# Performance work log

Hardware: AMD Instinct MI355X
Metric: run time of the kernel (lower is better)

The kernel has to match this reference:

```python
import jax, jax.numpy as jnp
import numpy as np

N_NODE = 1_000_000
N_BOND = 100_000
K_TWIST = 40
MAX_ORDER = 8
N_DOMAIN = 10_000
SIGMA_MAX = float(np.pi)  # config.sigma_max (=1) * pi


def setup_inputs() -> dict:
    key = jax.random.key(0)
    k1, k2, k3, k4, k5 = jax.random.split(key, 5)
    pos = jax.random.normal(k1, (N_NODE, 3), jnp.float32) * 10.0
    info_level = jax.random.uniform(k2, (N_BOND,), jnp.float32)
    # bond annotation: [order, u, v]
    uv = jax.random.randint(k3, (N_BOND, 2), 0, N_NODE, dtype=jnp.int32)
    order = (jnp.arange(N_BOND, dtype=jnp.int32) % MAX_ORDER)
    tor_bonds_anno = jnp.concatenate([order[:, None], uv], axis=1)
    # twisted nodes: bond b (order b%MAX_ORDER, group g=b//MAX_ORDER) twists
    # nodes g*K_TWIST .. g*K_TWIST+K_TWIST-1  -> disjoint within each order level
    b = jnp.arange(N_BOND, dtype=jnp.int32)
    nodes = (b // MAX_ORDER)[:, None] * K_TWIST + jnp.arange(K_TWIST, dtype=jnp.int32)[None, :]
    index_tor = jnp.repeat(b, K_TWIST)
    twisted_nodes_anno = jnp.stack([index_tor, nodes.reshape(-1)], axis=1)
    # rigid domains: contiguous blocks of nodes
    node_index = jnp.arange(N_NODE, dtype=jnp.int32)
    domain_index = node_index // (N_NODE // N_DOMAIN)
    eps = jax.random.normal(k4, (N_BOND,), jnp.float32)
    uniform_angles = jax.random.uniform(k5, (N_BOND,), jnp.float32, minval=-np.pi, maxval=np.pi)
    return {
        "pos": pos, "info_level": info_level,
        "tor_bonds_anno": tor_bonds_anno, "twisted_nodes_anno": twisted_nodes_anno,
        "domain_index": domain_index, "node_index": node_index,
        "eps": eps, "uniform_angles": uniform_angles, "from_prior": 1,
    }


def _rodrigues(axis, angle):
    # axis: [B,3] unit vectors, angle: [B] -> R: [B,3,3]
    c = jnp.cos(angle)[:, None, None]
    s = jnp.sin(angle)[:, None, None]
    ax, ay, az = axis[:, 0], axis[:, 1], axis[:, 2]
    zero = jnp.zeros_like(ax)
    K = jnp.stack([
        jnp.stack([zero, -az, ay], -1),
        jnp.stack([az, zero, -ax], -1),
        jnp.stack([-ay, ax, zero], -1),
    ], axis=1)  # [B,3,3]
    aaT = axis[:, :, None] * axis[:, None, :]
    I = jnp.eye(3, dtype=axis.dtype)[None]
    return c * I + s * K + (1.0 - c) * aaT


def _torsion_and_kabsch(pos, info_level, eps, uniform_angles,
                        tor_bonds_anno, twisted_nodes_anno,
                        domain_index, node_index, from_prior):
    tor_order = tor_bonds_anno[:, 0]
    u, v = tor_bonds_anno[:, 1], tor_bonds_anno[:, 2]
    index_tor = twisted_nodes_anno[:, 0]
    tnodes = twisted_nodes_anno[:, 1]

    sigmas = (1.0 - info_level) * SIGMA_MAX
    angles_wn = eps * sigmas  # wrapped-normal sample (rotation is 2pi-periodic)
    if from_prior:
        angles = jnp.where(info_level == 0, uniform_angles, angles_wn)
    else:
        angles = angles_wn

    pos_tor = pos
    # sequential application by torsion order (axes move as parents rotate)
    for o in range(MAX_ORDER):
        axis_raw = pos_tor[v] - pos_tor[u]
        axis = axis_raw / (jnp.linalg.norm(axis_raw, axis=-1, keepdims=True) + 1e-12)
        R = _rodrigues(axis, angles)                      # [n_bond,3,3]
        pivot = pos_tor[v]                                # rotate about atom v on the axis
        p = pos_tor[tnodes] - pivot[index_tor]            # [n_twisted,3]
        rot = jnp.einsum('nij,nj->ni', R[index_tor], p) + pivot[index_tor]
        mask = (tor_order[index_tor] == o)[:, None]
        delta = jnp.where(mask, rot - pos_tor[tnodes], 0.0)
        pos_tor = pos_tor.at[tnodes].add(delta)

    # decouple: per-domain Kabsch alignment of pos_tor back onto pos
    P = pos_tor[node_index]
    Q = pos[node_index]
    cnt = jax.ops.segment_sum(jnp.ones((P.shape[0],), P.dtype), domain_index, N_DOMAIN)[:, None]
    cP = jax.ops.segment_sum(P, domain_index, N_DOMAIN) / cnt
    cQ = jax.ops.segment_sum(Q, domain_index, N_DOMAIN) / cnt
    Pc = P - cP[domain_index]
    Qc = Q - cQ[domain_index]
    H = jax.ops.segment_sum(Pc[:, :, None] * Qc[:, None, :], domain_index, N_DOMAIN)  # [D,3,3]
    Uh, S, Vt = jnp.linalg.svd(H)
    V = jnp.swapaxes(Vt, 1, 2)
    d = jnp.sign(jnp.linalg.det(jnp.matmul(V, jnp.swapaxes(Uh, 1, 2))))  # [D]
    Vm = jnp.concatenate([V[:, :, :2], V[:, :, 2:] * d[:, None, None]], axis=2)
    Rg = jnp.matmul(Vm, jnp.swapaxes(Uh, 1, 2))            # [D,3,3], Rg @ p ~ q
    tg = cQ - jnp.einsum('dij,dj->di', Rg, cP)             # [D,3]
    corrected = jnp.einsum('nij,nj->ni', Rg[domain_index], P) + tg[domain_index]
    return pos_tor.at[node_index].set(corrected)


def reference(pos, info_level, tor_bonds_anno, twisted_nodes_anno,
              domain_index, node_index, eps, uniform_angles, from_prior):
    return _torsion_and_kabsch(pos, info_level, eps, uniform_angles,
                               tor_bonds_anno, twisted_nodes_anno,
                               domain_index, node_index, from_prior)
```

## Files before the change

kernel.cpp:

```cpp
#include <hip/hip_runtime.h>
#include <math.h>

#define N_NODE    1000000
#define N_BOND    100000
#define K_TWIST   40
#define MAX_ORDER 8
#define N_DOMAIN  10000
#define N_PER_DOM 100
#define N_GROUP   12500
#define N_TWIST   500000
#define SIGMA_MAXF 3.14159265358979323846f


#define M0_OFF  1500000
#define M1_OFF  1650000
#define BP_OFF  1800000

__global__ __launch_bounds__(256) void gather_k(
    const float* __restrict__ pos, const float* __restrict__ info_level,
    const int* __restrict__ anno, const float* __restrict__ eps,
    const float* __restrict__ uni, const int* __restrict__ from_prior_p,
    float* __restrict__ out)
{
    int b = blockIdx.x * 256 + threadIdx.x;
    if (b >= N_BOND) return;
    int o = b & (MAX_ORDER - 1);
    int u = anno[3*b + 1];
    int v = anno[3*b + 2];
    float info = info_level[b];
    float ang  = eps[b] * (1.0f - info) * SIGMA_MAXF;
    if (from_prior_p[0] != 0 && info == 0.0f) ang = uni[b];
    float4 r0, r1, r2;
    r0.x = pos[3*u+0]; r0.y = pos[3*u+1]; r0.z = pos[3*u+2];
    r0.w = pos[3*v+0]; r1.x = pos[3*v+1]; r1.y = pos[3*v+2];
    r1.z = cosf(ang);  r1.w = sinf(ang);
    r2.x = (u < N_TWIST) ? (float)(u / K_TWIST) : -1.0f;
    r2.y = (v < N_TWIST) ? (float)(v / K_TWIST) : -1.0f;
    r2.z = (anno[3*b] == o) ? 1.0f : 0.0f;
    r2.w = 0.0f;
    float4* bp4 = (float4*)(out + BP_OFF);
    bp4[3*b + 0] = r0;
    bp4[3*b + 1] = r1;
    bp4[3*b + 2] = r2;
}

__global__ __launch_bounds__(256) void compose_k(float* __restrict__ out, int o)
{
    int g = blockIdx.x * 256 + threadIdx.x;
    if (g >= N_GROUP) return;
    const float4* bp4 = (const float4*)(out + BP_OFF);
    const float* Mp = out + ((o & 1) ? M0_OFF : M1_OFF);
    float*       Mc = out + ((o & 1) ? M1_OFF : M0_OFF);
    int b = g * MAX_ORDER + o;
    float4 r0 = bp4[3*b + 0];
    float4 r1 = bp4[3*b + 1];
    float4 r2 = bp4[3*b + 2];
    float* mg = Mc + 12 * g;
    if (r2.z == 0.0f) {
        if (o == 0) {
            mg[0]=1.f; mg[1]=0.f; mg[2]=0.f;
            mg[3]=0.f; mg[4]=1.f; mg[5]=0.f;
            mg[6]=0.f; mg[7]=0.f; mg[8]=1.f;
            mg[9]=0.f; mg[10]=0.f; mg[11]=0.f;
        } else {
            const float* mp = Mp + 12 * g;
            #pragma unroll
            for (int k = 0; k < 12; k++) mg[k] = mp[k];
        }
        return;
    }
    float pu0 = r0.x, pu1 = r0.y, pu2 = r0.z;
    float pv0 = r0.w, pv1 = r1.x, pv2 = r1.y;
    float c = r1.z, s = r1.w;
    if (o > 0) {
        int gu = (int)r2.x;
        int gv = (int)r2.y;
        if (gu >= 0) {
            const float* m = Mp + 12 * gu;
            float a0 = m[0]*pu0 + m[1]*pu1 + m[2]*pu2 + m[9];
            float a1 = m[3]*pu0 + m[4]*pu1 + m[5]*pu2 + m[10];
            float a2 = m[6]*pu0 + m[7]*pu1 + m[8]*pu2 + m[11];
            pu0 = a0; pu1 = a1; pu2 = a2;
        }
        if (gv >= 0) {
            const float* m = Mp + 12 * gv;
            float a0 = m[0]*pv0 + m[1]*pv1 + m[2]*pv2 + m[9];
            float a1 = m[3]*pv0 + m[4]*pv1 + m[5]*pv2 + m[10];
            float a2 = m[6]*pv0 + m[7]*pv1 + m[8]*pv2 + m[11];
            pv0 = a0; pv1 = a1; pv2 = a2;
        }
    }
    float ax = pv0-pu0, ay = pv1-pu1, az = pv2-pu2;
    float inv = 1.0f / (sqrtf(ax*ax + ay*ay + az*az) + 1e-12f);
    ax *= inv; ay *= inv; az *= inv;
    float t = 1.0f - c;
    float R00 = c + t*ax*ax,     R01 = -s*az + t*ax*ay, R02 =  s*ay + t*ax*az;
    float R10 =  s*az + t*ay*ax, R11 = c + t*ay*ay,     R12 = -s*ax + t*ay*az;
    float R20 = -s*ay + t*az*ax, R21 =  s*ax + t*az*ay, R22 = c + t*az*az;
    if (o == 0) {
        mg[0]=R00; mg[1]=R01; mg[2]=R02;
        mg[3]=R10; mg[4]=R11; mg[5]=R12;
        mg[6]=R20; mg[7]=R21; mg[8]=R22;
        mg[9]  = pv0 - (R00*pv0 + R01*pv1 + R02*pv2);
        mg[10] = pv1 - (R10*pv0 + R11*pv1 + R12*pv2);
        mg[11] = pv2 - (R20*pv0 + R21*pv1 + R22*pv2);
    } else {
        const float* mp = Mp + 12 * g;
        mg[0] = R00*mp[0] + R01*mp[3] + R02*mp[6];
        mg[1] = R00*mp[1] + R01*mp[4] + R02*mp[7];
        mg[2] = R00*mp[2] + R01*mp[5] + R02*mp[8];
        mg[3] = R10*mp[0] + R11*mp[3] + R12*mp[6];
        mg[4] = R10*mp[1] + R11*mp[4] + R12*mp[7];
        mg[5] = R10*mp[2] + R11*mp[5] + R12*mp[8];
        mg[6] = R20*mp[0] + R21*mp[3] + R22*mp[6];
        mg[7] = R20*mp[1] + R21*mp[4] + R22*mp[7];
        mg[8] = R20*mp[2] + R21*mp[5] + R22*mp[8];
        float d0 = mp[9]-pv0, d1 = mp[10]-pv1, d2 = mp[11]-pv2;
        mg[9]  = R00*d0 + R01*d1 + R02*d2 + pv0;
        mg[10] = R10*d0 + R11*d1 + R12*d2 + pv1;
        mg[11] = R20*d0 + R21*d1 + R22*d2 + pv2;
    }
}

__device__ inline void cross3d(const double a[3], const double b[3], double r[3])
{
    r[0] = a[1]*b[2] - a[2]*b[1];
    r[1] = a[2]*b[0] - a[0]*b[2];
    r[2] = a[0]*b[1] - a[1]*b[0];
}

__device__ void kabsch_from_sums(const float* s, float* __restrict__ rt)
{
    const double inv_n = 1.0 / (double)N_PER_DOM;
    double sP[3] = { s[0], s[1], s[2] };
    double sQ[3] = { s[3], s[4], s[5] };
    double H[3][3];
    #pragma unroll
    for (int i = 0; i < 3; i++)
        #pragma unroll
        for (int j = 0; j < 3; j++)
            H[i][j] = (double)s[6 + 3*i + j] - sP[i]*sQ[j]*inv_n;
    double A[3][3];
    #pragma unroll
    for (int i = 0; i < 3; i++)
        #pragma unroll
        for (int j = 0; j < 3; j++)
            A[i][j] = H[0][i]*H[0][j] + H[1][i]*H[1][j] + H[2][i]*H[2][j];
    double V[3][3] = {{1,0,0},{0,1,0},{0,0,1}};
    for (int sweep = 0; sweep < 30; sweep++) {
        double off = A[0][1]*A[0][1] + A[0][2]*A[0][2] + A[1][2]*A[1][2];
        double n2  = A[0][0]*A[0][0] + A[1][1]*A[1][1] + A[2][2]*A[2][2];
        if (off <= 1e-28 * n2) break;
        for (int pp = 0; pp < 3; pp++) {
            int p = (pp == 2) ? 1 : 0;
            int q = (pp == 0) ? 1 : 2;
            double apq = A[p][q];
            if (apq == 0.0) continue;
            double tau = (A[q][q] - A[p][p]) / (2.0 * apq);
            double tj  = (tau >= 0.0 ? 1.0 : -1.0) / (fabs(tau) + sqrt(1.0 + tau*tau));
            double cj  = 1.0 / sqrt(1.0 + tj*tj);
            double sj  = tj * cj;
            int r = 3 - p - q;
            double app = A[p][p], aqq = A[q][q];
            A[p][p] = app - tj*apq;
            A[q][q] = aqq + tj*apq;
            A[p][q] = 0.0; A[q][p] = 0.0;
            double arp = A[r][p], arq = A[r][q];
            A[r][p] = cj*arp - sj*arq; A[p][r] = A[r][p];
            A[r][q] = sj*arp + cj*arq; A[q][r] = A[r][q];
            #pragma unroll
            for (int k = 0; k < 3; k++) {
                double vp = V[k][p], vq = V[k][q];
                V[k][p] = cj*vp - sj*vq;
                V[k][q] = sj*vp + cj*vq;
            }
        }
    }
    double wv[3] = { A[0][0], A[1][1], A[2][2] };
    int i0 = 0, i1 = 1, i2 = 2;
    if (wv[i0] < wv[i1]) { int t = i0; i0 = i1; i1 = t; }
    if (wv[i0] < wv[i2]) { int t = i0; i0 = i2; i2 = t; }
    if (wv[i1] < wv[i2]) { int t = i1; i1 = i2; i2 = t; }
    double v0[3] = { V[0][i0], V[1][i0], V[2][i0] };
    double v1[3] = { V[0][i1], V[1][i1], V[2][i1] };
    double v2[3] = { V[0][i2], V[1][i2], V[2][i2] };
    double s0 = sqrt(fmax(wv[i0], 0.0));
    double Rg[3][3];
    if (s0 < 1e-200) {
        Rg[0][0]=1; Rg[0][1]=0; Rg[0][2]=0;
        Rg[1][0]=0; Rg[1][1]=1; Rg[1][2]=0;
        Rg[2][0]=0; Rg[2][1]=0; Rg[2][2]=1;
    } else {
        double u0[3], u1[3], u2[3];
        #pragma unroll
        for (int i = 0; i < 3; i++)
            u0[i] = H[i][0]*v0[0] + H[i][1]*v0[1] + H[i][2]*v0[2];
        double n0 = sqrt(u0[0]*u0[0] + u0[1]*u0[1] + u0[2]*u0[2]);
        if (n0 > 0.0) { u0[0]/=n0; u0[1]/=n0; u0[2]/=n0; }
        else { u0[0]=1; u0[1]=0; u0[2]=0; }
        #pragma unroll
        for (int i = 0; i < 3; i++)
            u1[i] = H[i][0]*v1[0] + H[i][1]*v1[1] + H[i][2]*v1[2];
        double dp = u0[0]*u1[0] + u0[1]*u1[1] + u0[2]*u1[2];
        u1[0] -= dp*u0[0]; u1[1] -= dp*u0[1]; u1[2] -= dp*u0[2];
        double n1 = sqrt(u1[0]*u1[0] + u1[1]*u1[1] + u1[2]*u1[2]);
        if (n1 > 1e-12 * n0) { u1[0]/=n1; u1[1]/=n1; u1[2]/=n1; }
        else {
            double tv[3] = { (fabs(u0[0]) < 0.9) ? 1.0 : 0.0,
                             (fabs(u0[0]) < 0.9) ? 0.0 : 1.0, 0.0 };
            cross3d(u0, tv, u1);
            double nn = sqrt(u1[0]*u1[0] + u1[1]*u1[1] + u1[2]*u1[2]);
            u1[0]/=nn; u1[1]/=nn; u1[2]/=nn;
        }
        cross3d(u0, u1, u2);
        double c12[3]; cross3d(v1, v2, c12);
        double detV = v0[0]*c12[0] + v0[1]*c12[1] + v0[2]*c12[2];
        double dsg = (detV >= 0.0) ? 1.0 : -1.0;
        #pragma unroll
        for (int r = 0; r < 3; r++)
            #pragma unroll
            for (int c = 0; c < 3; c++)
                Rg[r][c] = v0[r]*u0[c] + v1[r]*u1[c] + dsg*v2[r]*u2[c];
    }
    double cP[3] = { sP[0]*inv_n, sP[1]*inv_n, sP[2]*inv_n };
    double cQ[3] = { sQ[0]*inv_n, sQ[1]*inv_n, sQ[2]*inv_n };
    #pragma unroll
    for (int i = 0; i < 3; i++) {
        rt[3*i+0] = (float)Rg[i][0];
        rt[3*i+1] = (float)Rg[i][1];
        rt[3*i+2] = (float)Rg[i][2];
        rt[9+i] = (float)(cQ[i] - (Rg[i][0]*cP[0] + Rg[i][1]*cP[1] + Rg[i][2]*cP[2]));
    }
}

__device__ inline void acc15(float a[15], float p0, float p1, float p2,
                             float q0, float q1, float q2)
{
    a[0]+=p0;    a[1]+=p1;    a[2]+=p2;
    a[3]+=q0;    a[4]+=q1;    a[5]+=q2;
    a[6]+=p0*q0; a[7]+=p0*q1; a[8]+=p0*q2;
    a[9]+=p1*q0; a[10]+=p1*q1;a[11]+=p1*q2;
    a[12]+=p2*q0;a[13]+=p2*q1;a[14]+=p2*q2;
}

__global__ __launch_bounds__(256) void rsvd_k(const float* __restrict__ pos,
                                              const float* __restrict__ out,
                                              float* __restrict__ rt)
{
    int d = blockIdx.x * 256 + threadIdx.x;
    if (d >= N_DOMAIN) return;
    const float4* pv4 = (const float4*)pos;
    const float* Mf = out + M1_OFF;
    float a[15];
    #pragma unroll
    for (int k = 0; k < 15; k++) a[k] = 0.f;

    if (d >= N_TWIST / N_PER_DOM) {
        int base = 75 * d;
        for (int c = 0; c < 25; c++) {
            float4 f0 = pv4[base + 3*c + 0];
            float4 f1 = pv4[base + 3*c + 1];
            float4 f2 = pv4[base + 3*c + 2];
            acc15(a, f0.x, f0.y, f0.z, f0.x, f0.y, f0.z);
            acc15(a, f0.w, f1.x, f1.y, f0.w, f1.x, f1.y);
            acc15(a, f1.z, f1.w, f2.x, f1.z, f1.w, f2.x);
            acc15(a, f2.y, f2.z, f2.w, f2.y, f2.z, f2.w);
        }
    } else {
        int n = d * N_PER_DOM, end = n + N_PER_DOM;
        while (n < end) {
            int g = n / K_TWIST;
            int segEnd = min(end, K_TWIST * (g + 1));
            const float* m = Mf + 12 * g;
            float m0=m[0],m1=m[1],m2=m[2],m3=m[3],m4=m[4],m5=m[5];
            float m6=m[6],m7=m[7],m8=m[8],m9=m[9],m10=m[10],m11=m[11];
            int chunks = (segEnd - n) >> 2;
            int base = (3 * n) >> 2;
            for (int c = 0; c < chunks; c++) {
                float4 f0 = pv4[base + 3*c + 0];
                float4 f1 = pv4[base + 3*c + 1];
                float4 f2 = pv4[base + 3*c + 2];
                float q0, q1, q2, p0, p1, p2;
                q0=f0.x; q1=f0.y; q2=f0.z;
                p0=m0*q0+m1*q1+m2*q2+m9; p1=m3*q0+m4*q1+m5*q2+m10; p2=m6*q0+m7*q1+m8*q2+m11;
                acc15(a, p0, p1, p2, q0, q1, q2);
                q0=f0.w; q1=f1.x; q2=f1.y;
                p0=m0*q0+m1*q1+m2*q2+m9; p1=m3*q0+m4*q1+m5*q2+m10; p2=m6*q0+m7*q1+m8*q2+m11;
                acc15(a, p0, p1, p2, q0, q1, q2);
                q0=f1.z; q1=f1.w; q2=f2.x;
                p0=m0*q0+m1*q1+m2*q2+m9; p1=m3*q0+m4*q1+m5*q2+m10; p2=m6*q0+m7*q1+m8*q2+m11;
                acc15(a, p0, p1, p2, q0, q1, q2);
                q0=f2.y; q1=f2.z; q2=f2.w;
                p0=m0*q0+m1*q1+m2*q2+m9; p1=m3*q0+m4*q1+m5*q2+m10; p2=m6*q0+m7*q1+m8*q2+m11;
                acc15(a, p0, p1, p2, q0, q1, q2);
            }
            n = segEnd;
        }
    }
    kabsch_from_sums(a, rt + (size_t)d * 12);
}

__global__ void apply_low_k(const float* __restrict__ pos,
                            const float* __restrict__ rt,
                            float* __restrict__ out)
{
    int n = blockIdx.x * 256 + threadIdx.x;
    if (n >= N_TWIST) return;
    const float* m = out + M1_OFF + 12 * (n / K_TWIST);
    const float* w = rt + 12 * (n / N_PER_DOM);
    float q0 = pos[3*n+0], q1 = pos[3*n+1], q2 = pos[3*n+2];
    float p0 = m[0]*q0 + m[1]*q1 + m[2]*q2 + m[9];
    float p1 = m[3]*q0 + m[4]*q1 + m[5]*q2 + m[10];
    float p2 = m[6]*q0 + m[7]*q1 + m[8]*q2 + m[11];
    out[3*n+0] = w[0]*p0 + w[1]*p1 + w[2]*p2 + w[9];
    out[3*n+1] = w[3]*p0 + w[4]*p1 + w[5]*p2 + w[10];
    out[3*n+2] = w[6]*p0 + w[7]*p1 + w[8]*p2 + w[11];
}

__global__ void apply_high_k(const float* __restrict__ pos,
                             const float* __restrict__ rt,
                             float* __restrict__ out)
{
    int i = blockIdx.x * 256 + threadIdx.x;
    int n = N_TWIST + i;
    if (n >= N_NODE) return;
    const float* w = rt + 12 * (n / N_PER_DOM);
    float q0 = pos[3*n+0], q1 = pos[3*n+1], q2 = pos[3*n+2];
    out[3*n+0] = w[0]*q0 + w[1]*q1 + w[2]*q2 + w[9];
    out[3*n+1] = w[3]*q0 + w[4]*q1 + w[5]*q2 + w[10];
    out[3*n+2] = w[6]*q0 + w[7]*q1 + w[8]*q2 + w[11];
}

extern "C" void kernel_launch(void* const* d_in, const int* in_sizes, int n_in,
                              void* d_out, int out_size, void* d_ws, size_t ws_size,
                              hipStream_t stream)
{
    const float* pos        = (const float*)d_in[0];
    const float* info_level = (const float*)d_in[1];
    const int*   anno       = (const int*)  d_in[2];
    const float* eps        = (const float*)d_in[6];
    const float* uni        = (const float*)d_in[7];
    const int*   from_prior = (const int*)  d_in[8];
    float* out = (float*)d_out;
    float* rt  = (float*)d_ws;

    gather_k<<<(N_BOND + 255)/256, 256, 0, stream>>>(
        pos, info_level, anno, eps, uni, from_prior, out);

    for (int o = 0; o < MAX_ORDER; o++)
        compose_k<<<(N_GROUP + 255)/256, 256, 0, stream>>>(out, o);

    rsvd_k<<<(N_DOMAIN + 255)/256, 256, 0, stream>>>(pos, out, rt);

    apply_low_k<<<(N_TWIST + 255)/256, 256, 0, stream>>>(pos, rt, out);
    apply_high_k<<<(N_NODE - N_TWIST + 255)/256, 256, 0, stream>>>(pos, rt, out);
}
```

Baseline: 186.3 us.

## Fuse per-order compose launches into one dataflow kernel with spin flags

Replaces the eight sequential compose kernel launches with a single kernel in which each group thread iterates over all orders. Cross-group dependencies are resolved through per-group progress flags, spin-waited with atomics, and each order level's matrices are stored in a separate buffer. This removes seven launches and their inter-kernel gaps, at the cost of atomic traffic and a deadlock risk if dependent groups are not co-resident. The buffer layout moves to per-level storage, and the final level feeds the downstream kernels.

Result: slower. 205.7 us (+10.4%).

```diff
diff --git a/kernel.cpp b/kernel.cpp
--- a/kernel.cpp
+++ b/kernel.cpp
@@ -12,18 +12,21 @@
 #define SIGMA_MAXF 3.14159265358979323846f
 
 
-#define M0_OFF  1500000
-#define M1_OFF  1650000
-#define BP_OFF  1800000
+#define BP_OFF   0
+#define MLV_OFF  1500000
+#define MLV_STRIDE 150000
+#define RT_WORDS 120000
+#define SPIN_MAX 100000000
 
 __global__ __launch_bounds__(256) void gather_k(
     const float* __restrict__ pos, const float* __restrict__ info_level,
     const int* __restrict__ anno, const float* __restrict__ eps,
     const float* __restrict__ uni, const int* __restrict__ from_prior_p,
-    float* __restrict__ out)
+    float* __restrict__ out, unsigned int* __restrict__ flags)
 {
     int b = blockIdx.x * 256 + threadIdx.x;
     if (b >= N_BOND) return;
+    if (b < N_GROUP) atomicExch(&flags[b], 0u);
     int o = b & (MAX_ORDER - 1);
     int u = anno[3*b + 1];
     int v = anno[3*b + 2];
@@ -44,81 +47,122 @@
     bp4[3*b + 2] = r2;
 }
 
-__global__ __launch_bounds__(256) void compose_k(float* __restrict__ out, int o)
+__device__ inline unsigned long long pack2f(float a, float b)
+{
+    return ((unsigned long long)__float_as_uint(b) << 32) | __float_as_uint(a);
+}
+
+__device__ inline void unpack2f(unsigned long long w, float* a, float* b)
+{
+    *a = __uint_as_float((unsigned int)(w & 0xffffffffull));
+    *b = __uint_as_float((unsigned int)(w >> 32));
+}
+
+__device__ inline void spin_flag(unsigned int* f, unsigned int need)
+{
+    for (int it = 0; it < SPIN_MAX; ++it)
+        if (atomicAdd(f, 0u) >= need) return;
+}
+
+__device__ inline void read_M(unsigned long long* mp, float m[12])
+{
+    unsigned long long w0 = atomicAdd(&mp[0], 0ull);
+    unsigned long long w1 = atomicAdd(&mp[1], 0ull);
+    unsigned long long w2 = atomicAdd(&mp[2], 0ull);
+    unsigned long long w3 = atomicAdd(&mp[3], 0ull);
+    unsigned long long w4 = atomicAdd(&mp[4], 0ull);
+    unsigned long long w5 = atomicAdd(&mp[5], 0ull);
+    unpack2f(w0, &m[0], &m[1]);  unpack2f(w1, &m[2], &m[3]);
+    unpack2f(w2, &m[4], &m[5]);  unpack2f(w3, &m[6], &m[7]);
+    unpack2f(w4, &m[8], &m[9]);  unpack2f(w5, &m[10], &m[11]);
+}
+
+__global__ __launch_bounds__(256) void compose_df_k(float* __restrict__ out,
+                                                    unsigned int* __restrict__ flags)
 {
     int g = blockIdx.x * 256 + threadIdx.x;
     if (g >= N_GROUP) return;
     const float4* bp4 = (const float4*)(out + BP_OFF);
-    const float* Mp = out + ((o & 1) ? M0_OFF : M1_OFF);
-    float*       Mc = out + ((o & 1) ? M1_OFF : M0_OFF);
-    int b = g * MAX_ORDER + o;
-    float4 r0 = bp4[3*b + 0];
-    float4 r1 = bp4[3*b + 1];
-    float4 r2 = bp4[3*b + 2];
-    float* mg = Mc + 12 * g;
-    if (r2.z == 0.0f) {
-        if (o == 0) {
-            mg[0]=1.f; mg[1]=0.f; mg[2]=0.f;
-            mg[3]=0.f; mg[4]=1.f; mg[5]=0.f;
-            mg[6]=0.f; mg[7]=0.f; mg[8]=1.f;
-            mg[9]=0.f; mg[10]=0.f; mg[11]=0.f;
-        } else {
-            const float* mp = Mp + 12 * g;
-            #pragma unroll
-            for (int k = 0; k < 12; k++) mg[k] = mp[k];
+    float M[12];
+    for (int o = 0; o < MAX_ORDER; o++) {
+        int b = g * MAX_ORDER + o;
+        float4 r0 = bp4[3*b + 0];
+        float4 r1 = bp4[3*b + 1];
+        float4 r2 = bp4[3*b + 2];
+        if (r2.z != 0.0f) {
+            float pu0 = r0.x, pu1 = r0.y, pu2 = r0.z;
+            float pv0 = r0.w, pv1 = r1.x, pv2 = r1.y;
+            float c = r1.z, s = r1.w;
+            if (o > 0) {
+                int gu = (int)r2.x;
+                int gv = (int)r2.y;
+                unsigned long long* Mprev =
+                    (unsigned long long*)(out + MLV_OFF + (size_t)(o-1) * MLV_STRIDE);
+                if (gu >= 0) {
+                    spin_flag(&flags[gu], (unsigned int)o);
+                    float m[12];
+                    read_M(Mprev + 6 * gu, m);
+                    float a0 = m[0]*pu0 + m[1]*pu1 + m[2]*pu2 + m[9];
+                    float a1 = m[3]*pu0 + m[4]*pu1 + m[5]*pu2 + m[10];
+                    float a2 = m[6]*pu0 + m[7]*pu1 + m[8]*pu2 + m[11];
+                    pu0 = a0; pu1 = a1; pu2 = a2;
+                }
+                if (gv >= 0) {
+                    spin_flag(&flags[gv], (unsigned int)o);
+                    float m[12];
+                    read_M(Mprev + 6 * gv, m);
+                    float a0 = m[0]*pv0 + m[1]*pv1 + m[2]*pv2 + m[9];
+                    float a1 = m[3]*pv0 + m[4]*pv1 + m[5]*pv2 + m[10];
+                    float a2 = m[6]*pv0 + m[7]*pv1 + m[8]*pv2 + m[11];
+                    pv0 = a0; pv1 = a1; pv2 = a2;
+                }
+            }
+            float ax = pv0-pu0, ay = pv1-pu1, az = pv2-pu2;
+            float inv = 1.0f / (sqrtf(ax*ax + ay*ay + az*az) + 1e-12f);
+            ax *= inv; ay *= inv; az *= inv;
+            float t = 1.0f - c;
+            float R00 = c + t*ax*ax,     R01 = -s*az + t*ax*ay, R02 =  s*ay + t*ax*az;
+            float R10 =  s*az + t*ay*ax, R11 = c + t*ay*ay,     R12 = -s*ax + t*ay*az;
+            float R20 = -s*ay + t*az*ax, R21 =  s*ax + t*az*ay, R22 = c + t*az*az;
+            if (o == 0) {
+                M[0]=R00; M[1]=R01; M[2]=R02;
+                M[3]=R10; M[4]=R11; M[5]=R12;
+                M[6]=R20; M[7]=R21; M[8]=R22;
+                M[9]  = pv0 - (R00*pv0 + R01*pv1 + R02*pv2);
+                M[10] = pv1 - (R10*pv0 + R11*pv1 + R12*pv2);
+                M[11] = pv2 - (R20*pv0 + R21*pv1 + R22*pv2);
+            } else {
+                float n0 = R00*M[0] + R01*M[3] + R02*M[6];
+                float n1 = R00*M[1] + R01*M[4] + R02*M[7];
+                float n2 = R00*M[2] + R01*M[5] + R02*M[8];
+                float n3 = R10*M[0] + R11*M[3] + R12*M[6];
+                float n4 = R10*M[1] + R11*M[4] + R12*M[7];
+                float n5 = R10*M[2] + R11*M[5] + R12*M[8];
+                float n6 = R20*M[0] + R21*M[3] + R22*M[6];
+                float n7 = R20*M[1] + R21*M[4] + R22*M[7];
+                float n8 = R20*M[2] + R21*M[5] + R22*M[8];
+                float d0 = M[9]-pv0, d1 = M[10]-pv1, d2 = M[11]-pv2;
+                float n9  = R00*d0 + R01*d1 + R02*d2 + pv0;
+                float n10 = R10*d0 + R11*d1 + R12*d2 + pv1;
+                float n11 = R20*d0 + R21*d1 + R22*d2 + pv2;
+                M[0]=n0; M[1]=n1; M[2]=n2; M[3]=n3; M[4]=n4; M[5]=n5;
+                M[6]=n6; M[7]=n7; M[8]=n8; M[9]=n9; M[10]=n10; M[11]=n11;
+            }
+        } else if (o == 0) {
+            M[0]=1.f; M[1]=0.f; M[2]=0.f; M[3]=0.f; M[4]=1.f; M[5]=0.f;
+            M[6]=0.f; M[7]=0.f; M[8]=1.f; M[9]=0.f; M[10]=0.f; M[11]=0.f;
         }
-        return;
-    }
-    float pu0 = r0.x, pu1 = r0.y, pu2 = r0.z;
-    float pv0 = r0.w, pv1 = r1.x, pv2 = r1.y;
-    float c = r1.z, s = r1.w;
-    if (o > 0) {
-        int gu = (int)r2.x;
-        int gv = (int)r2.y;
-        if (gu >= 0) {
-            const float* m = Mp + 12 * gu;
-            float a0 = m[0]*pu0 + m[1]*pu1 + m[2]*pu2 + m[9];
-            float a1 = m[3]*pu0 + m[4]*pu1 + m[5]*pu2 + m[10];
-            float a2 = m[6]*pu0 + m[7]*pu1 + m[8]*pu2 + m[11];
-            pu0 = a0; pu1 = a1; pu2 = a2;
-        }
-        if (gv >= 0) {
-            const float* m = Mp + 12 * gv;
-            float a0 = m[0]*pv0 + m[1]*pv1 + m[2]*pv2 + m[9];
-            float a1 = m[3]*pv0 + m[4]*pv1 + m[5]*pv2 + m[10];
-            float a2 = m[6]*pv0 + m[7]*pv1 + m[8]*pv2 + m[11];
-            pv0 = a0; pv1 = a1; pv2 = a2;
-        }
-    }
-    float ax = pv0-pu0, ay = pv1-pu1, az = pv2-pu2;
-    float inv = 1.0f / (sqrtf(ax*ax + ay*ay + az*az) + 1e-12f);
-    ax *= inv; ay *= inv; az *= inv;
-    float t = 1.0f - c;
-    float R00 = c + t*ax*ax,     R01 = -s*az + t*ax*ay, R02 =  s*ay + t*ax*az;
-    float R10 =  s*az + t*ay*ax, R11 = c + t*ay*ay,     R12 = -s*ax + t*ay*az;
-    float R20 = -s*ay + t*az*ax, R21 =  s*ax + t*az*ay, R22 = c + t*az*az;
-    if (o == 0) {
-        mg[0]=R00; mg[1]=R01; mg[2]=R02;
-        mg[3]=R10; mg[4]=R11; mg[5]=R12;
-        mg[6]=R20; mg[7]=R21; mg[8]=R22;
-        mg[9]  = pv0 - (R00*pv0 + R01*pv1 + R02*pv2);
-        mg[10] = pv1 - (R10*pv0 + R11*pv1 + R12*pv2);
-        mg[11] = pv2 - (R20*pv0 + R21*pv1 + R22*pv2);
-    } else {
-        const float* mp = Mp + 12 * g;
-        mg[0] = R00*mp[0] + R01*mp[3] + R02*mp[6];
-        mg[1] = R00*mp[1] + R01*mp[4] + R02*mp[7];
-        mg[2] = R00*mp[2] + R01*mp[5] + R02*mp[8];
-        mg[3] = R10*mp[0] + R11*mp[3] + R12*mp[6];
-        mg[4] = R10*mp[1] + R11*mp[4] + R12*mp[7];
-        mg[5] = R10*mp[2] + R11*mp[5] + R12*mp[8];
-        mg[6] = R20*mp[0] + R21*mp[3] + R22*mp[6];
-        mg[7] = R20*mp[1] + R21*mp[4] + R22*mp[7];
-        mg[8] = R20*mp[2] + R21*mp[5] + R22*mp[8];
-        float d0 = mp[9]-pv0, d1 = mp[10]-pv1, d2 = mp[11]-pv2;
-        mg[9]  = R00*d0 + R01*d1 + R02*d2 + pv0;
-        mg[10] = R10*d0 + R11*d1 + R12*d2 + pv1;
-        mg[11] = R20*d0 + R21*d1 + R22*d2 + pv2;
+
+        unsigned long long* mp =
+            (unsigned long long*)(out + MLV_OFF + (size_t)o * MLV_STRIDE) + 6 * g;
+        atomicExch(&mp[0], pack2f(M[0], M[1]));
+        atomicExch(&mp[1], pack2f(M[2], M[3]));
+        atomicExch(&mp[2], pack2f(M[4], M[5]));
+        atomicExch(&mp[3], pack2f(M[6], M[7]));
+        atomicExch(&mp[4], pack2f(M[8], M[9]));
+        atomicExch(&mp[5], pack2f(M[10], M[11]));
+        __threadfence();
+        atomicExch(&flags[g], (unsigned int)(o + 1));
     }
 }
 
@@ -250,7 +294,7 @@
     int d = blockIdx.x * 256 + threadIdx.x;
     if (d >= N_DOMAIN) return;
     const float4* pv4 = (const float4*)pos;
-    const float* Mf = out + M1_OFF;
+    const float* Mf = out + MLV_OFF + 7 * MLV_STRIDE;
     float a[15];
     #pragma unroll
     for (int k = 0; k < 15; k++) a[k] = 0.f;
@@ -306,7 +350,7 @@
 {
     int n = blockIdx.x * 256 + threadIdx.x;
     if (n >= N_TWIST) return;
-    const float* m = out + M1_OFF + 12 * (n / K_TWIST);
+    const float* m = out + MLV_OFF + 7 * MLV_STRIDE + 12 * (n / K_TWIST);
     const float* w = rt + 12 * (n / N_PER_DOM);
     float q0 = pos[3*n+0], q1 = pos[3*n+1], q2 = pos[3*n+2];
     float p0 = m[0]*q0 + m[1]*q1 + m[2]*q2 + m[9];
@@ -343,12 +387,12 @@
     const int*   from_prior = (const int*)  d_in[8];
     float* out = (float*)d_out;
     float* rt  = (float*)d_ws;
+    unsigned int* flags = (unsigned int*)((char*)d_ws + 480000);
 
     gather_k<<<(N_BOND + 255)/256, 256, 0, stream>>>(
-        pos, info_level, anno, eps, uni, from_prior, out);
-
-    for (int o = 0; o < MAX_ORDER; o++)
-        compose_k<<<(N_GROUP + 255)/256, 256, 0, stream>>>(out, o);
+        pos, info_level, anno, eps, uni, from_prior, out, flags);
+
+    compose_df_k<<<(N_GROUP + 255)/256, 256, 0, stream>>>(out, flags);
 
     rsvd_k<<<(N_DOMAIN + 255)/256, 256, 0, stream>>>(pos, out, rt);
 
```

## Fuse bond gather into compose and fold final order into consumers

Applied to the files above, without the earlier changes.

Removes the separate bond-parameter gather kernel, so each compose pass reads anno, pos and angle inputs directly and computes cos/sin only for active bonds. The last compose launch (order 7) is dropped; its transform is recomputed on the fly inside rsvd_k and apply_low_k from the order-6 matrices. rsvd_k now uses 64-thread blocks to spread the 10k domain threads over more blocks. This saves two launches and the staging buffer traffic, at the cost of redundant order-7 recomputation (one per node in apply_low_k) and heavier per-thread register use in rsvd_k.

After: 192.5 us. +3.3%, slower.

```diff
diff --git a/kernel.cpp b/kernel.cpp
--- a/kernel.cpp
+++ b/kernel.cpp
@@ -12,51 +12,22 @@
 #define SIGMA_MAXF 3.14159265358979323846f
 
 
-#define M0_OFF  1500000
-#define M1_OFF  1650000
-#define BP_OFF  1800000
-
-__global__ __launch_bounds__(256) void gather_k(
+#define TA_OFF  1500000
+#define TB_OFF  1650000
+
+__global__ __launch_bounds__(256) void compose_k(
     const float* __restrict__ pos, const float* __restrict__ info_level,
     const int* __restrict__ anno, const float* __restrict__ eps,
     const float* __restrict__ uni, const int* __restrict__ from_prior_p,
-    float* __restrict__ out)
-{
-    int b = blockIdx.x * 256 + threadIdx.x;
-    if (b >= N_BOND) return;
-    int o = b & (MAX_ORDER - 1);
-    int u = anno[3*b + 1];
-    int v = anno[3*b + 2];
-    float info = info_level[b];
-    float ang  = eps[b] * (1.0f - info) * SIGMA_MAXF;
-    if (from_prior_p[0] != 0 && info == 0.0f) ang = uni[b];
-    float4 r0, r1, r2;
-    r0.x = pos[3*u+0]; r0.y = pos[3*u+1]; r0.z = pos[3*u+2];
-    r0.w = pos[3*v+0]; r1.x = pos[3*v+1]; r1.y = pos[3*v+2];
-    r1.z = cosf(ang);  r1.w = sinf(ang);
-    r2.x = (u < N_TWIST) ? (float)(u / K_TWIST) : -1.0f;
-    r2.y = (v < N_TWIST) ? (float)(v / K_TWIST) : -1.0f;
-    r2.z = (anno[3*b] == o) ? 1.0f : 0.0f;
-    r2.w = 0.0f;
-    float4* bp4 = (float4*)(out + BP_OFF);
-    bp4[3*b + 0] = r0;
-    bp4[3*b + 1] = r1;
-    bp4[3*b + 2] = r2;
-}
-
-__global__ __launch_bounds__(256) void compose_k(float* __restrict__ out, int o)
+    float* __restrict__ out, int o)
 {
     int g = blockIdx.x * 256 + threadIdx.x;
     if (g >= N_GROUP) return;
-    const float4* bp4 = (const float4*)(out + BP_OFF);
-    const float* Mp = out + ((o & 1) ? M0_OFF : M1_OFF);
-    float*       Mc = out + ((o & 1) ? M1_OFF : M0_OFF);
+    const float* Mp = out + ((o & 1) ? TA_OFF : TB_OFF);
+    float*       Mc = out + ((o & 1) ? TB_OFF : TA_OFF);
     int b = g * MAX_ORDER + o;
-    float4 r0 = bp4[3*b + 0];
-    float4 r1 = bp4[3*b + 1];
-    float4 r2 = bp4[3*b + 2];
     float* mg = Mc + 12 * g;
-    if (r2.z == 0.0f) {
+    if (anno[3*b] != o) {
         if (o == 0) {
             mg[0]=1.f; mg[1]=0.f; mg[2]=0.f;
             mg[3]=0.f; mg[4]=1.f; mg[5]=0.f;
@@ -69,31 +40,33 @@
         }
         return;
     }
-    float pu0 = r0.x, pu1 = r0.y, pu2 = r0.z;
-    float pv0 = r0.w, pv1 = r1.x, pv2 = r1.y;
-    float c = r1.z, s = r1.w;
+    int u = anno[3*b + 1];
+    int v = anno[3*b + 2];
+    float pu0 = pos[3*u+0], pu1 = pos[3*u+1], pu2 = pos[3*u+2];
+    float pv0 = pos[3*v+0], pv1 = pos[3*v+1], pv2 = pos[3*v+2];
     if (o > 0) {
-        int gu = (int)r2.x;
-        int gv = (int)r2.y;
-        if (gu >= 0) {
-            const float* m = Mp + 12 * gu;
+        if (u < N_TWIST) {
+            const float* m = Mp + 12 * (u / K_TWIST);
             float a0 = m[0]*pu0 + m[1]*pu1 + m[2]*pu2 + m[9];
             float a1 = m[3]*pu0 + m[4]*pu1 + m[5]*pu2 + m[10];
             float a2 = m[6]*pu0 + m[7]*pu1 + m[8]*pu2 + m[11];
             pu0 = a0; pu1 = a1; pu2 = a2;
         }
-        if (gv >= 0) {
-            const float* m = Mp + 12 * gv;
+        if (v < N_TWIST) {
+            const float* m = Mp + 12 * (v / K_TWIST);
             float a0 = m[0]*pv0 + m[1]*pv1 + m[2]*pv2 + m[9];
             float a1 = m[3]*pv0 + m[4]*pv1 + m[5]*pv2 + m[10];
             float a2 = m[6]*pv0 + m[7]*pv1 + m[8]*pv2 + m[11];
             pv0 = a0; pv1 = a1; pv2 = a2;
         }
     }
+    float info = info_level[b];
+    float ang  = eps[b] * (1.0f - info) * SIGMA_MAXF;
+    if (from_prior_p[0] != 0 && info == 0.0f) ang = uni[b];
     float ax = pv0-pu0, ay = pv1-pu1, az = pv2-pu2;
     float inv = 1.0f / (sqrtf(ax*ax + ay*ay + az*az) + 1e-12f);
     ax *= inv; ay *= inv; az *= inv;
-    float t = 1.0f - c;
+    float c = cosf(ang), s = sinf(ang), t = 1.0f - c;
     float R00 = c + t*ax*ax,     R01 = -s*az + t*ax*ay, R02 =  s*ay + t*ax*az;
     float R10 =  s*az + t*ay*ax, R11 = c + t*ay*ay,     R12 = -s*ax + t*ay*az;
     float R20 = -s*ay + t*az*ax, R21 =  s*ax + t*az*ay, R22 = c + t*az*az;
@@ -120,6 +93,64 @@
         mg[10] = R10*d0 + R11*d1 + R12*d2 + pv1;
         mg[11] = R20*d0 + R21*d1 + R22*d2 + pv2;
     }
+}
+
+__device__ void final_M(const float* __restrict__ M6S,
+                        const float* __restrict__ pos,
+                        const float* __restrict__ info_level,
+                        const int* __restrict__ anno,
+                        const float* __restrict__ eps,
+                        const float* __restrict__ uni,
+                        int from_prior, int g, float Mf[12])
+{
+    const float* mp = M6S + 12 * g;
+    int b = g * MAX_ORDER + 7;
+    if (anno[3*b] != 7) {
+        #pragma unroll
+        for (int k = 0; k < 12; k++) Mf[k] = mp[k];
+        return;
+    }
+    int u = anno[3*b + 1];
+    int v = anno[3*b + 2];
+    float pu0 = pos[3*u+0], pu1 = pos[3*u+1], pu2 = pos[3*u+2];
+    float pv0 = pos[3*v+0], pv1 = pos[3*v+1], pv2 = pos[3*v+2];
+    if (u < N_TWIST) {
+        const float* m = M6S + 12 * (u / K_TWIST);
+        float a0 = m[0]*pu0 + m[1]*pu1 + m[2]*pu2 + m[9];
+        float a1 = m[3]*pu0 + m[4]*pu1 + m[5]*pu2 + m[10];
+        float a2 = m[6]*pu0 + m[7]*pu1 + m[8]*pu2 + m[11];
+        pu0 = a0; pu1 = a1; pu2 = a2;
+    }
+    if (v < N_TWIST) {
+        const float* m = M6S + 12 * (v / K_TWIST);
+        float a0 = m[0]*pv0 + m[1]*pv1 + m[2]*pv2 + m[9];
+        float a1 = m[3]*pv0 + m[4]*pv1 + m[5]*pv2 + m[10];
+        float a2 = m[6]*pv0 + m[7]*pv1 + m[8]*pv2 + m[11];
+        pv0 = a0; pv1 = a1; pv2 = a2;
+    }
+    float info = info_level[b];
+    float ang  = eps[b] * (1.0f - info) * SIGMA_MAXF;
+    if (from_prior != 0 && info == 0.0f) ang = uni[b];
+    float ax = pv0-pu0, ay = pv1-pu1, az = pv2-pu2;
+    float inv = 1.0f / (sqrtf(ax*ax + ay*ay + az*az) + 1e-12f);
+    ax *= inv; ay *= inv; az *= inv;
+    float c = cosf(ang), s = sinf(ang), t = 1.0f - c;
+    float R00 = c + t*ax*ax,     R01 = -s*az + t*ax*ay, R02 =  s*ay + t*ax*az;
+    float R10 =  s*az + t*ay*ax, R11 = c + t*ay*ay,     R12 = -s*ax + t*ay*az;
+    float R20 = -s*ay + t*az*ax, R21 =  s*ax + t*az*ay, R22 = c + t*az*az;
+    Mf[0] = R00*mp[0] + R01*mp[3] + R02*mp[6];
+    Mf[1] = R00*mp[1] + R01*mp[4] + R02*mp[7];
+    Mf[2] = R00*mp[2] + R01*mp[5] + R02*mp[8];
+    Mf[3] = R10*mp[0] + R11*mp[3] + R12*mp[6];
+    Mf[4] = R10*mp[1] + R11*mp[4] + R12*mp[7];
+    Mf[5] = R10*mp[2] + R11*mp[5] + R12*mp[8];
+    Mf[6] = R20*mp[0] + R21*mp[3] + R22*mp[6];
+    Mf[7] = R20*mp[1] + R21*mp[4] + R22*mp[7];
+    Mf[8] = R20*mp[2] + R21*mp[5] + R22*mp[8];
+    float d0 = mp[9]-pv0, d1 = mp[10]-pv1, d2 = mp[11]-pv2;
+    Mf[9]  = R00*d0 + R01*d1 + R02*d2 + pv0;
+    Mf[10] = R10*d0 + R11*d1 + R12*d2 + pv1;
+    Mf[11] = R20*d0 + R21*d1 + R22*d2 + pv2;
 }
 
 __device__ inline void cross3d(const double a[3], const double b[3], double r[3])
@@ -243,14 +274,15 @@
     a[12]+=p2*q0;a[13]+=p2*q1;a[14]+=p2*q2;
 }
 
-__global__ __launch_bounds__(256) void rsvd_k(const float* __restrict__ pos,
-                                              const float* __restrict__ out,
-                                              float* __restrict__ rt)
-{
-    int d = blockIdx.x * 256 + threadIdx.x;
+__global__ __launch_bounds__(64) void rsvd_k(
+    const float* __restrict__ pos, const float* __restrict__ info_level,
+    const int* __restrict__ anno, const float* __restrict__ eps,
+    const float* __restrict__ uni, const int* __restrict__ from_prior_p,
+    const float* __restrict__ out, float* __restrict__ rt)
+{
+    int d = blockIdx.x * 64 + threadIdx.x;
     if (d >= N_DOMAIN) return;
     const float4* pv4 = (const float4*)pos;
-    const float* Mf = out + M1_OFF;
     float a[15];
     #pragma unroll
     for (int k = 0; k < 15; k++) a[k] = 0.f;
@@ -267,11 +299,19 @@
             acc15(a, f2.y, f2.z, f2.w, f2.y, f2.z, f2.w);
         }
     } else {
+        const float* M6S = out + TA_OFF;
+        int g0 = (100 * d) / K_TWIST;
+        float Mg[3][12];
+        int from_prior = from_prior_p[0];
+        #pragma unroll
+        for (int j = 0; j < 3; j++)
+            final_M(M6S, pos, info_level, anno, eps, uni, from_prior,
+                    g0 + j, Mg[j]);
         int n = d * N_PER_DOM, end = n + N_PER_DOM;
         while (n < end) {
-            int g = n / K_TWIST;
-            int segEnd = min(end, K_TWIST * (g + 1));
-            const float* m = Mf + 12 * g;
+            int gseg = n / K_TWIST;
+            int segEnd = min(end, K_TWIST * (gseg + 1));
+            const float* m = Mg[gseg - g0];
             float m0=m[0],m1=m[1],m2=m[2],m3=m[3],m4=m[4],m5=m[5];
             float m6=m[6],m7=m[7],m8=m[8],m9=m[9],m10=m[10],m11=m[11];
             int chunks = (segEnd - n) >> 2;
@@ -300,13 +340,17 @@
     kabsch_from_sums(a, rt + (size_t)d * 12);
 }
 
-__global__ void apply_low_k(const float* __restrict__ pos,
-                            const float* __restrict__ rt,
-                            float* __restrict__ out)
+__global__ __launch_bounds__(256) void apply_low_k(
+    const float* __restrict__ pos, const float* __restrict__ info_level,
+    const int* __restrict__ anno, const float* __restrict__ eps,
+    const float* __restrict__ uni, const int* __restrict__ from_prior_p,
+    const float* __restrict__ rt, float* __restrict__ out)
 {
     int n = blockIdx.x * 256 + threadIdx.x;
     if (n >= N_TWIST) return;
-    const float* m = out + M1_OFF + 12 * (n / K_TWIST);
+    float m[12];
+    final_M(out + TA_OFF, pos, info_level, anno, eps, uni, from_prior_p[0],
+            n / K_TWIST, m);
     const float* w = rt + 12 * (n / N_PER_DOM);
     float q0 = pos[3*n+0], q1 = pos[3*n+1], q2 = pos[3*n+2];
     float p0 = m[0]*q0 + m[1]*q1 + m[2]*q2 + m[9];
@@ -317,9 +361,9 @@
     out[3*n+2] = w[6]*p0 + w[7]*p1 + w[8]*p2 + w[11];
 }
 
-__global__ void apply_high_k(const float* __restrict__ pos,
-                             const float* __restrict__ rt,
-                             float* __restrict__ out)
+__global__ __launch_bounds__(256) void apply_high_k(
+    const float* __restrict__ pos, const float* __restrict__ rt,
+    float* __restrict__ out)
 {
     int i = blockIdx.x * 256 + threadIdx.x;
     int n = N_TWIST + i;
@@ -344,14 +388,14 @@
     float* out = (float*)d_out;
     float* rt  = (float*)d_ws;
 
-    gather_k<<<(N_BOND + 255)/256, 256, 0, stream>>>(
-        pos, info_level, anno, eps, uni, from_prior, out);
-
-    for (int o = 0; o < MAX_ORDER; o++)
-        compose_k<<<(N_GROUP + 255)/256, 256, 0, stream>>>(out, o);
-
-    rsvd_k<<<(N_DOMAIN + 255)/256, 256, 0, stream>>>(pos, out, rt);
-
-    apply_low_k<<<(N_TWIST + 255)/256, 256, 0, stream>>>(pos, rt, out);
+    for (int o = 0; o < 7; o++)
+        compose_k<<<(N_GROUP + 255)/256, 256, 0, stream>>>(
+            pos, info_level, anno, eps, uni, from_prior, out, o);
+
+    rsvd_k<<<(N_DOMAIN + 63)/64, 64, 0, stream>>>(
+        pos, info_level, anno, eps, uni, from_prior, out, rt);
+
+    apply_low_k<<<(N_TWIST + 255)/256, 256, 0, stream>>>(
+        pos, info_level, anno, eps, uni, from_prior, rt, out);
     apply_high_k<<<(N_NODE - N_TWIST + 255)/256, 256, 0, stream>>>(pos, rt, out);
 }
```
